# Performance work log

Hardware: AMD Instinct MI355X
Metric: run time of the kernel (lower is better)

## Reference

```python
import jax, jax.numpy as jnp
import numpy as np

B, CQ, CKV, E = 8, 256, 256, 256
H, W = 64, 64
HP, WP = 32, 32


def setup_inputs() -> dict:
    key = jax.random.key(0)
    ks = jax.random.split(key, 6)
    C = jax.random.normal(ks[0], (B, CQ, H, W), dtype=jnp.float32)
    P = jax.random.normal(ks[1], (B, CKV, HP, WP), dtype=jnp.float32)
    # 1x1 conv weights, kaiming-ish scale; stored as [out_ch, in_ch]
    theta_w = jax.random.normal(ks[2], (E, CQ), dtype=jnp.float32) * (1.0 / np.sqrt(CQ))
    phi_w = jax.random.normal(ks[3], (E, CKV), dtype=jnp.float32) * (1.0 / np.sqrt(CKV))
    g_w = jax.random.normal(ks[4], (E, CKV), dtype=jnp.float32) * (1.0 / np.sqrt(CKV))
    out_w = jax.random.normal(ks[5], (CQ, E), dtype=jnp.float32) * (1.0 / np.sqrt(E))
    return {"C": C, "P": P, "theta_w": theta_w, "phi_w": phi_w, "g_w": g_w, "out_w": out_w}


def reference(C, P, theta_w, phi_w, g_w, out_w):
    b, _, h, w = C.shape
    e = theta_w.shape[0]
    # 1x1 convs are channel GEMMs
    theta_C = jnp.einsum('bchw,ec->behw', C, theta_w).reshape(b, e, h * w)   # [B,E,Nq]
    phi_P = jnp.einsum('bchw,ec->behw', P, phi_w).reshape(b, e, -1)          # [B,E,Nkv]
    g_P = jnp.einsum('bchw,ec->behw', P, g_w).reshape(b, e, -1)              # [B,E,Nkv]
    attn = jnp.einsum('ben,bem->bnm', theta_C, phi_P) / (e ** 0.5)           # [B,Nq,Nkv]
    attn = jax.nn.softmax(attn, axis=-1)
    out = jnp.einsum('bem,bnm->ben', g_P, attn).reshape(b, e, h, w)          # [B,E,H,W]
    out = jnp.einsum('behw,ce->bchw', out, out_w)                            # [B,CQ,H,W]
    return jnp.concatenate([C, out], axis=1)
```

## Files before the change

kernel.cpp:

```cpp
#include <hip/hip_runtime.h>


typedef __attribute__((ext_vector_type(8))) short short8;
typedef __attribute__((ext_vector_type(16))) float f32x16;
typedef unsigned short ushort_t;

__device__ __forceinline__ unsigned short f2bf(float f) {
    unsigned int u = __float_as_uint(f);
    u += 0x7FFFu + ((u >> 16) & 1u);
    return (unsigned short)(u >> 16);
}
__device__ __forceinline__ unsigned int pack2bf(float a, float b) {
    return (unsigned int)f2bf(a) | ((unsigned int)f2bf(b) << 16);
}
__device__ __forceinline__ void gload16(const ushort_t* g, ushort_t* l) {
    __builtin_amdgcn_global_load_lds(
        (const __attribute__((address_space(1))) unsigned int*)g,
        (__attribute__((address_space(3))) unsigned int*)l, 16, 0, 0);
}
__device__ __forceinline__ f32x16 zero16() {
    f32x16 z;
#pragma unroll
    for (int i = 0; i < 16; ++i) z[i] = 0.f;
    return z;
}

__global__ __launch_bounds__(256) void prep_w(const float* __restrict__ thw,
                                              const float* __restrict__ phw,
                                              const float* __restrict__ ow,
                                              const float* __restrict__ gw,
                                              ushort_t* __restrict__ thc,
                                              ushort_t* __restrict__ phc,
                                              ushort_t* __restrict__ w2c) {
    int blk = blockIdx.x;
    int t = threadIdx.x;
    if (blk < 64) {
        int which = blk >> 5;
        int e0 = (blk & 31) * 8;
        const float* src = which ? phw : thw;
        ushort_t* dst = which ? phc : thc;
#pragma unroll
        for (int i = 0; i < 8; ++i) {
            int e = e0 + i, c = t;
            int idx = ((((e >> 5) * 16 + (c >> 4)) * 64 + ((c >> 3) & 1) * 32 + (e & 31)) << 3) + (c & 7);
            dst[idx] = f2bf(src[e * 256 + c]);
        }
    } else {
        int c0 = (blk - 64) * 8;
        float acc[8] = {};
        for (int e = 0; e < 256; ++e) {
            float g = gw[e * 256 + t];
#pragma unroll
            for (int i = 0; i < 8; ++i) acc[i] += ow[(c0 + i) * 256 + e] * g;
        }
#pragma unroll
        for (int i = 0; i < 8; ++i) {
            int c = c0 + i, k = t;
            int idx = ((((c >> 5) * 16 + (k >> 4)) * 64 + ((k >> 3) & 1) * 32 + (c & 31)) << 3) + (k & 7);
            w2c[idx] = f2bf(acc[i]);
        }
    }
}

__global__ __launch_bounds__(256, 4) void proj_all(const ushort_t* __restrict__ thc,
                                                   const ushort_t* __restrict__ phc,
                                                   const ushort_t* __restrict__ w2c,
                                                   const float* __restrict__ C,
                                                   const float* __restrict__ P,
                                                   ushort_t* __restrict__ thetaA,
                                                   ushort_t* __restrict__ phiA,
                                                   ushort_t* __restrict__ gVx) {
    __shared__ __align__(16) ushort_t Xc[16384];
    int blk = blockIdx.x;
    int tid = threadIdx.x, lane = tid & 63, wid = tid >> 6;
    int l31 = lane & 31, lh = lane >> 5;
    const int wq = wid & 1, we = wid >> 1;

    int role, b, nt, N;
    const ushort_t* Wc;
    const float* Xg;
    ushort_t* outp;
    float scale = 1.f;
    if (blk < 512) {
        role = 0; b = blk & 7; nt = blk >> 3;
        Wc = thc; Xg = C + (size_t)b * 1048576; outp = thetaA + (size_t)b * 1048576;
        N = 4096; scale = 1.4426950408889634f / 16.0f;
    } else if (blk < 640) {
        int r = blk - 512; role = 1; b = r & 7; nt = r >> 3;
        Wc = phc; Xg = P + (size_t)b * 262144; outp = phiA + (size_t)b * 262144;
        N = 1024;
    } else {
        int r = blk - 640; role = 2; b = r & 7; nt = r >> 3;
        Wc = w2c; Xg = P + (size_t)b * 262144; outp = gVx + (size_t)b * 262144;
        N = 1024;
    }

    {
        const float* Xb = Xg + nt * 64;
        const int q = lane;
        const int sq = q >> 5, sl = q & 31;
#pragma unroll
        for (int it = 0; it < 16; ++it) {
            int ch0 = wid * 4 + it * 16;
            float v0 = Xb[(size_t)(ch0 + 0) * N + q];
            float v1 = Xb[(size_t)(ch0 + 1) * N + q];
            float v2 = Xb[(size_t)(ch0 + 2) * N + q];
            float v3 = Xb[(size_t)(ch0 + 3) * N + q];
            uint2 w;
            w.x = pack2bf(v0, v1);
            w.y = pack2bf(v2, v3);
            int ks = ch0 >> 4;
            int slh = (ch0 >> 3) & 1;
            size_t a = ((size_t)(ks * 2 + sq) * 64 + slh * 32 + sl) * 8 + (ch0 & 7);
            *(uint2*)&Xc[a] = w;
        }
    }
    __syncthreads();

    const int n0 = nt * 64 + wq * 32;
    const int ncr = (n0 >> 5) * 16;

    f32x16 o[4];
#pragma unroll
    for (int f = 0; f < 4; ++f) o[f] = zero16();

#pragma unroll
    for (int ks = 0; ks < 16; ++ks) {
        short8 xf = *(const short8*)(Xc + ((size_t)(ks * 2 + wq) * 64 + lane) * 8);
#pragma unroll
        for (int f2 = 0; f2 < 4; ++f2) {
            int f = we * 4 + f2;
            short8 wf = *(const short8*)(Wc + ((size_t)(f * 16 + ks) * 64 + lane) * 8);
            o[f2] = __builtin_amdgcn_mfma_f32_32x32x16_bf16(wf, xf, o[f2], 0, 0, 0);
        }
    }

    if (role < 2) {
#pragma unroll
        for (int f2 = 0; f2 < 4; ++f2) {
            int f = we * 4 + f2;
#pragma unroll
            for (int rq = 0; rq < 4; ++rq) {
                uint2 st;
                st.x = pack2bf(o[f2][4 * rq + 0] * scale, o[f2][4 * rq + 1] * scale);
                st.y = pack2bf(o[f2][4 * rq + 2] * scale, o[f2][4 * rq + 3] * scale);
                size_t addr = ((size_t)(ncr + f * 2 + (rq >> 1)) * 64 + l31 + 32 * (rq & 1)) * 8 + 4 * lh;
                *(uint2*)(outp + addr) = st;
            }
        }
    } else {
        int kvq = (n0 >> 4) + (l31 >> 4);
        int lhw = 32 * ((l31 >> 3) & 1);
        int kl = l31 & 7;
#pragma unroll
        for (int f2 = 0; f2 < 4; ++f2) {
            int f = we * 4 + f2;
#pragma unroll
            for (int r2 = 0; r2 < 16; ++r2) {
                int crow = (r2 & 3) + 8 * (r2 >> 2) + 4 * lh;
                size_t addr = ((size_t)(f * 64 + kvq) * 64 + crow + lhw) * 8 + kl;
                outp[addr] = f2bf(o[f2][r2]);
            }
        }
    }
}

__global__ __launch_bounds__(512, 2) void attn14(const ushort_t* __restrict__ thetaA,
                                                 const ushort_t* __restrict__ phiA,
                                                 const ushort_t* __restrict__ gVx,
                                                 const float* __restrict__ Cf,
                                                 float* __restrict__ out) {
    const int b = blockIdx.x & 7, qt = blockIdx.x >> 3;
    const int tid = threadIdx.x, lane = tid & 63, wid = tid >> 6;
    const int l31 = lane & 31, lh = lane >> 5;
    const int qg = wid & 3, z = wid >> 2;

    __shared__ __align__(16) ushort_t smem[65536];
    __shared__ __align__(16) ushort_t Pl[2][8192];

    const ushort_t* thA = thetaA + (size_t)b * 1048576;
    const ushort_t* phA = phiA + (size_t)b * 262144;
    const ushort_t* gVb = gVx + (size_t)b * 262144;

    auto stageK = [&](int j) {
        if (wid < 4) {
            const ushort_t* src = phA + (size_t)j * 16384 + (size_t)wid * 4096 + lane * 8;
            ushort_t* dst = smem + (j & 1) * 16384 + wid * 4096;
#pragma unroll
            for (int i = 0; i < 8; ++i) gload16(src + i * 512, dst + i * 512);
        }
    };
    auto stageV = [&](int j) {
        if (wid >= 4) {
            int w = wid - 4;
#pragma unroll
            for (int q2 = 0; q2 < 2; ++q2) {
                int f = w * 2 + q2;
#pragma unroll
                for (int jj = 0; jj < 4; ++jj) {
                    const ushort_t* src = gVb + ((size_t)(f * 64 + j * 4 + jj) * 64 + lane) * 8;
                    ushort_t* dst = smem + 32768 + (j & 1) * 16384 + f * 2048 + jj * 512;
                    gload16(src, dst);
                }
            }
        }
    };

    stageK(0); stageV(0);

    short8 qf[16];
    {
        const int qcr = (qt * 4 + qg) * 16;
#pragma unroll
        for (int ks = 0; ks < 16; ++ks)
            qf[ks] = *(const short8*)(thA + ((size_t)(qcr + ks) * 64 + lane) * 8);
    }

    asm volatile("s_waitcnt vmcnt(0)" ::: "memory");
    __builtin_amdgcn_s_barrier();
    __builtin_amdgcn_sched_barrier(0);
    stageK(1);

    f32x16 s = zero16();
    {
        const ushort_t* Kb = smem + z * 8192;
#pragma unroll
        for (int ks = 0; ks < 16; ++ks) {
            short8 kf = *(const short8*)(Kb + (size_t)ks * 512 + lane * 8);
            s = __builtin_amdgcn_mfma_f32_32x32x16_bf16(kf, qf[ks], s, 0, 0, 0);
        }
    }

    f32x16 o[4];
#pragma unroll
    for (int f = 0; f < 4; ++f) o[f] = zero16();
    float rl = 0.f;

    const size_t cbase = (size_t)b * 1048576 + (size_t)qt * 128 + (size_t)l31 * 4;
    const size_t dofs = (size_t)b * 1048576;
    size_t cpo = 0;
    float4 cpv;

    for (int it = 0; it < 16; ++it) {
#pragma unroll
        for (int r = 0; r < 16; ++r) s[r] = __builtin_amdgcn_exp2f(s[r]);
        float t0 = (s[0] + s[1]) + (s[2] + s[3]);
        float t1 = (s[4] + s[5]) + (s[6] + s[7]);
        float t2 = (s[8] + s[9]) + (s[10] + s[11]);
        float t3 = (s[12] + s[13]) + (s[14] + s[15]);
        float ps = (t0 + t1) + (t2 + t3);
        ps += __shfl_xor(ps, 32);
        rl += ps;

        unsigned int a0 = pack2bf(s[0], s[1]),   b0 = pack2bf(s[4], s[5]);
        unsigned int a1 = pack2bf(s[2], s[3]),   b1 = pack2bf(s[6], s[7]);
        unsigned int a2 = pack2bf(s[8], s[9]),   b2 = pack2bf(s[12], s[13]);
        unsigned int a3 = pack2bf(s[10], s[11]), b3 = pack2bf(s[14], s[15]);
        asm volatile("v_permlane32_swap_b32 %0, %1" : "+v"(a0), "+v"(b0));
        asm volatile("v_permlane32_swap_b32 %0, %1" : "+v"(a1), "+v"(b1));
        asm volatile("v_permlane32_swap_b32 %0, %1" : "+v"(a2), "+v"(b2));
        asm volatile("v_permlane32_swap_b32 %0, %1" : "+v"(a3), "+v"(b3));
        union PW { unsigned int u[4]; short8 v; };
        PW pw0, pw1;
        pw0.u[0] = a0; pw0.u[1] = a1; pw0.u[2] = b0; pw0.u[3] = b1;
        pw1.u[0] = a2; pw1.u[1] = a3; pw1.u[2] = b2; pw1.u[3] = b3;
        ushort_t* Pw = &Pl[it & 1][0];
        *(short8*)(Pw + ((size_t)(qg * 4 + 2 * z + 0) * 64 + lane) * 8) = pw0.v;
        *(short8*)(Pw + ((size_t)(qg * 4 + 2 * z + 1) * 64 + lane) * 8) = pw1.v;

        if (it == 0) asm volatile("s_waitcnt vmcnt(0)" ::: "memory");
        else         asm volatile("s_waitcnt vmcnt(1)" ::: "memory");
        asm volatile("s_waitcnt lgkmcnt(0)" ::: "memory");
        __builtin_amdgcn_s_barrier();
        __builtin_amdgcn_sched_barrier(0);

        if (it > 0) *(float4*)(out + cpo + dofs) = cpv;
        if (it < 14) stageK(it + 2);
        if (it < 15) stageV(it + 1);
        __builtin_amdgcn_sched_barrier(0);
        cpo = cbase + (size_t)(it * 16 + 2 * wid + lh) * 4096;
        cpv = *(const float4*)(Cf + cpo);

        const ushort_t* Vb = smem + 32768 + (it & 1) * 16384 + z * 8192;
        const ushort_t* Kb = smem + ((it + 1) & 1) * 16384 + z * 8192;
        const ushort_t* Pr = &Pl[it & 1][0];
        __builtin_amdgcn_s_setprio(1);
        if (it < 15) {
            f32x16 sn = zero16();
#pragma unroll
            for (int j = 0; j < 4; ++j) {
                short8 pf = *(const short8*)(Pr + ((size_t)(qg * 4 + j) * 64 + lane) * 8);
#pragma unroll
                for (int fl = 0; fl < 4; ++fl) {
                    short8 vf = *(const short8*)(Vb + (size_t)fl * 2048 + j * 512 + lane * 8);
                    o[fl] = __builtin_amdgcn_mfma_f32_32x32x16_bf16(vf, pf, o[fl], 0, 0, 0);
                    int ks = j * 4 + fl;
                    short8 kf = *(const short8*)(Kb + (size_t)ks * 512 + lane * 8);
                    sn = __builtin_amdgcn_mfma_f32_32x32x16_bf16(kf, qf[ks], sn, 0, 0, 0);
                }
            }
            s = sn;
        } else {
#pragma unroll
            for (int j = 0; j < 4; ++j) {
                short8 pf = *(const short8*)(Pr + ((size_t)(qg * 4 + j) * 64 + lane) * 8);
#pragma unroll
                for (int fl = 0; fl < 4; ++fl) {
                    short8 vf = *(const short8*)(Vb + (size_t)fl * 2048 + j * 512 + lane * 8);
                    o[fl] = __builtin_amdgcn_mfma_f32_32x32x16_bf16(vf, pf, o[fl], 0, 0, 0);
                }
            }
        }
        __builtin_amdgcn_s_setprio(0);
        __builtin_amdgcn_sched_barrier(0);
    }

    *(float4*)(out + cpo + dofs) = cpv;

    __syncthreads();
    float* rlS = (float*)smem;
    if (lane < 32) rlS[(z * 4 + qg) * 32 + l31] = rl;
    __syncthreads();
    float inv = 1.f / (rlS[(0 * 4 + qg) * 32 + l31] + rlS[(1 * 4 + qg) * 32 + l31]);
    float* ob = out + (size_t)b * 2097152 + (size_t)256 * 4096 + qt * 128 + qg * 32 + l31;
#pragma unroll
    for (int fl = 0; fl < 4; ++fl) {
#pragma unroll
        for (int r = 0; r < 16; ++r) {
            int e = z * 128 + fl * 32 + (r & 3) + 8 * (r >> 2) + 4 * lh;
            ob[(size_t)e * 4096] = o[fl][r] * inv;
        }
    }
}


extern "C" void kernel_launch(void* const* d_in, const int* in_sizes, int n_in,
                              void* d_out, int out_size, void* d_ws, size_t ws_size,
                              hipStream_t stream) {
    const float* C       = (const float*)d_in[0];
    const float* P       = (const float*)d_in[1];
    const float* theta_w = (const float*)d_in[2];
    const float* phi_w   = (const float*)d_in[3];
    const float* g_w     = (const float*)d_in[4];
    const float* out_w   = (const float*)d_in[5];
    float* out = (float*)d_out;

    ushort_t* ws = (ushort_t*)d_ws;
    ushort_t* thetaA = ws;
    ushort_t* phiA   = ws + 8388608;
    ushort_t* gVx    = ws + 10485760;
    ushort_t* thWc   = ws + 12582912;
    ushort_t* phWc   = ws + 12648448;
    ushort_t* w2c    = ws + 12713984;

    prep_w<<<96, 256, 0, stream>>>(theta_w, phi_w, out_w, g_w, thWc, phWc, w2c);
    proj_all<<<768, 256, 0, stream>>>(thWc, phWc, w2c, C, P, thetaA, phiA, gVx);
    attn14<<<256, 512, 0, stream>>>(thetaA, phiA, gVx, C, out);
}
```

Before: 103.8 us.

## Warp-specialize attention kernel with dedicated producer waves for loads and C copy

Adds four producer waves to the attention block, raising it to 768 threads. These waves alone issue the K/V global-to-LDS staging and the copy of the C passthrough channels. The eight compute waves now only do softmax and MFMA work, and the aim is to take load-issue and copy instructions off their critical path. In exchange, launch_bounds drops the min-2-blocks hint, so register budget and occupancy may change. Producer waves also wait with vmcnt(2) at each barrier, which can add stalls if their loads lag.

```diff
diff --git a/kernel.cpp b/kernel.cpp
--- a/kernel.cpp
+++ b/kernel.cpp
@@ -165,15 +165,16 @@
     }
 }
 
-__global__ __launch_bounds__(512, 2) void attn14(const ushort_t* __restrict__ thetaA,
-                                                 const ushort_t* __restrict__ phiA,
-                                                 const ushort_t* __restrict__ gVx,
-                                                 const float* __restrict__ Cf,
-                                                 float* __restrict__ out) {
+__global__ __launch_bounds__(768) void attn15(const ushort_t* __restrict__ thetaA,
+                                              const ushort_t* __restrict__ phiA,
+                                              const ushort_t* __restrict__ gVx,
+                                              const float* __restrict__ Cf,
+                                              float* __restrict__ out) {
     const int b = blockIdx.x & 7, qt = blockIdx.x >> 3;
     const int tid = threadIdx.x, lane = tid & 63, wid = tid >> 6;
     const int l31 = lane & 31, lh = lane >> 5;
-    const int qg = wid & 3, z = wid >> 2;
+    const bool comp = wid < 8;
+    const int qg = wid & 3, z = (wid >> 2) & 1;
 
     __shared__ __align__(16) ushort_t smem[65536];
     __shared__ __align__(16) ushort_t Pl[2][8192];
@@ -183,24 +184,26 @@
     const ushort_t* gVb = gVx + (size_t)b * 262144;
 
     auto stageK = [&](int j) {
-        if (wid < 4) {
-            const ushort_t* src = phA + (size_t)j * 16384 + (size_t)wid * 4096 + lane * 8;
-            ushort_t* dst = smem + (j & 1) * 16384 + wid * 4096;
-#pragma unroll
-            for (int i = 0; i < 8; ++i) gload16(src + i * 512, dst + i * 512);
+        if (wid == 8 || wid == 9) {
+            int w = wid - 8;
+#pragma unroll
+            for (int i = 0; i < 16; ++i) {
+                int ch = w * 16 + i;
+                gload16(phA + (size_t)j * 16384 + (size_t)ch * 512 + lane * 8,
+                        smem + (j & 1) * 16384 + ch * 512);
+            }
         }
     };
     auto stageV = [&](int j) {
-        if (wid >= 4) {
-            int w = wid - 4;
-#pragma unroll
-            for (int q2 = 0; q2 < 2; ++q2) {
-                int f = w * 2 + q2;
+        if (wid == 10 || wid == 11) {
+            int w = wid - 10;
+#pragma unroll
+            for (int q2 = 0; q2 < 4; ++q2) {
+                int f = w * 4 + q2;
 #pragma unroll
                 for (int jj = 0; jj < 4; ++jj) {
-                    const ushort_t* src = gVb + ((size_t)(f * 64 + j * 4 + jj) * 64 + lane) * 8;
-                    ushort_t* dst = smem + 32768 + (j & 1) * 16384 + f * 2048 + jj * 512;
-                    gload16(src, dst);
+                    gload16(gVb + ((size_t)(f * 64 + j * 4 + jj) * 64 + lane) * 8,
+                            smem + 32768 + (j & 1) * 16384 + f * 2048 + jj * 512);
                 }
             }
         }
@@ -209,7 +212,7 @@
     stageK(0); stageV(0);
 
     short8 qf[16];
-    {
+    if (comp) {
         const int qcr = (qt * 4 + qg) * 16;
 #pragma unroll
         for (int ks = 0; ks < 16; ++ks)
@@ -222,7 +225,7 @@
     stageK(1);
 
     f32x16 s = zero16();
-    {
+    if (comp) {
         const ushort_t* Kb = smem + z * 8192;
 #pragma unroll
         for (int ks = 0; ks < 16; ++ks) {
@@ -236,99 +239,116 @@
     for (int f = 0; f < 4; ++f) o[f] = zero16();
     float rl = 0.f;
 
-    const size_t cbase = (size_t)b * 1048576 + (size_t)qt * 128 + (size_t)l31 * 4;
+    const size_t cbase = (size_t)b * 1048576 + (size_t)qt * 128;
     const size_t dofs = (size_t)b * 1048576;
-    size_t cpo = 0;
-    float4 cpv;
+    size_t cpo0 = 0, cpo1 = 0;
+    float4 cpv0, cpv1;
 
     for (int it = 0; it < 16; ++it) {
-#pragma unroll
-        for (int r = 0; r < 16; ++r) s[r] = __builtin_amdgcn_exp2f(s[r]);
-        float t0 = (s[0] + s[1]) + (s[2] + s[3]);
-        float t1 = (s[4] + s[5]) + (s[6] + s[7]);
-        float t2 = (s[8] + s[9]) + (s[10] + s[11]);
-        float t3 = (s[12] + s[13]) + (s[14] + s[15]);
-        float ps = (t0 + t1) + (t2 + t3);
-        ps += __shfl_xor(ps, 32);
-        rl += ps;
-
-        unsigned int a0 = pack2bf(s[0], s[1]),   b0 = pack2bf(s[4], s[5]);
-        unsigned int a1 = pack2bf(s[2], s[3]),   b1 = pack2bf(s[6], s[7]);
-        unsigned int a2 = pack2bf(s[8], s[9]),   b2 = pack2bf(s[12], s[13]);
-        unsigned int a3 = pack2bf(s[10], s[11]), b3 = pack2bf(s[14], s[15]);
-        asm volatile("v_permlane32_swap_b32 %0, %1" : "+v"(a0), "+v"(b0));
-        asm volatile("v_permlane32_swap_b32 %0, %1" : "+v"(a1), "+v"(b1));
-        asm volatile("v_permlane32_swap_b32 %0, %1" : "+v"(a2), "+v"(b2));
-        asm volatile("v_permlane32_swap_b32 %0, %1" : "+v"(a3), "+v"(b3));
-        union PW { unsigned int u[4]; short8 v; };
-        PW pw0, pw1;
-        pw0.u[0] = a0; pw0.u[1] = a1; pw0.u[2] = b0; pw0.u[3] = b1;
-        pw1.u[0] = a2; pw1.u[1] = a3; pw1.u[2] = b2; pw1.u[3] = b3;
-        ushort_t* Pw = &Pl[it & 1][0];
-        *(short8*)(Pw + ((size_t)(qg * 4 + 2 * z + 0) * 64 + lane) * 8) = pw0.v;
-        *(short8*)(Pw + ((size_t)(qg * 4 + 2 * z + 1) * 64 + lane) * 8) = pw1.v;
-
-        if (it == 0) asm volatile("s_waitcnt vmcnt(0)" ::: "memory");
-        else         asm volatile("s_waitcnt vmcnt(1)" ::: "memory");
-        asm volatile("s_waitcnt lgkmcnt(0)" ::: "memory");
+        if (comp) {
+#pragma unroll
+            for (int r = 0; r < 16; ++r) s[r] = __builtin_amdgcn_exp2f(s[r]);
+            float t0 = (s[0] + s[1]) + (s[2] + s[3]);
+            float t1 = (s[4] + s[5]) + (s[6] + s[7]);
+            float t2 = (s[8] + s[9]) + (s[10] + s[11]);
+            float t3 = (s[12] + s[13]) + (s[14] + s[15]);
+            float ps = (t0 + t1) + (t2 + t3);
+            ps += __shfl_xor(ps, 32);
+            rl += ps;
+
+            unsigned int a0 = pack2bf(s[0], s[1]),   b0 = pack2bf(s[4], s[5]);
+            unsigned int a1 = pack2bf(s[2], s[3]),   b1 = pack2bf(s[6], s[7]);
+            unsigned int a2 = pack2bf(s[8], s[9]),   b2 = pack2bf(s[12], s[13]);
+            unsigned int a3 = pack2bf(s[10], s[11]), b3 = pack2bf(s[14], s[15]);
+            asm volatile("v_permlane32_swap_b32 %0, %1" : "+v"(a0), "+v"(b0));
+            asm volatile("v_permlane32_swap_b32 %0, %1" : "+v"(a1), "+v"(b1));
+            asm volatile("v_permlane32_swap_b32 %0, %1" : "+v"(a2), "+v"(b2));
+            asm volatile("v_permlane32_swap_b32 %0, %1" : "+v"(a3), "+v"(b3));
+            union PW { unsigned int u[4]; short8 v; };
+            PW pw0, pw1;
+            pw0.u[0] = a0; pw0.u[1] = a1; pw0.u[2] = b0; pw0.u[3] = b1;
+            pw1.u[0] = a2; pw1.u[1] = a3; pw1.u[2] = b2; pw1.u[3] = b3;
+            ushort_t* Pw = &Pl[it & 1][0];
+            *(short8*)(Pw + ((size_t)(qg * 4 + 2 * z + 0) * 64 + lane) * 8) = pw0.v;
+            *(short8*)(Pw + ((size_t)(qg * 4 + 2 * z + 1) * 64 + lane) * 8) = pw1.v;
+            asm volatile("s_waitcnt lgkmcnt(0)" ::: "memory");
+        } else {
+            if (it == 0) asm volatile("s_waitcnt vmcnt(0)" ::: "memory");
+            else         asm volatile("s_waitcnt vmcnt(2)" ::: "memory");
+        }
         __builtin_amdgcn_s_barrier();
         __builtin_amdgcn_sched_barrier(0);
 
-        if (it > 0) *(float4*)(out + cpo + dofs) = cpv;
-        if (it < 14) stageK(it + 2);
-        if (it < 15) stageV(it + 1);
-        __builtin_amdgcn_sched_barrier(0);
-        cpo = cbase + (size_t)(it * 16 + 2 * wid + lh) * 4096;
-        cpv = *(const float4*)(Cf + cpo);
-
-        const ushort_t* Vb = smem + 32768 + (it & 1) * 16384 + z * 8192;
-        const ushort_t* Kb = smem + ((it + 1) & 1) * 16384 + z * 8192;
-        const ushort_t* Pr = &Pl[it & 1][0];
-        __builtin_amdgcn_s_setprio(1);
-        if (it < 15) {
-            f32x16 sn = zero16();
-#pragma unroll
-            for (int j = 0; j < 4; ++j) {
-                short8 pf = *(const short8*)(Pr + ((size_t)(qg * 4 + j) * 64 + lane) * 8);
-#pragma unroll
-                for (int fl = 0; fl < 4; ++fl) {
-                    short8 vf = *(const short8*)(Vb + (size_t)fl * 2048 + j * 512 + lane * 8);
-                    o[fl] = __builtin_amdgcn_mfma_f32_32x32x16_bf16(vf, pf, o[fl], 0, 0, 0);
-                    int ks = j * 4 + fl;
-                    short8 kf = *(const short8*)(Kb + (size_t)ks * 512 + lane * 8);
-                    sn = __builtin_amdgcn_mfma_f32_32x32x16_bf16(kf, qf[ks], sn, 0, 0, 0);
+        if (comp) {
+            const ushort_t* Vb = smem + 32768 + (it & 1) * 16384 + z * 8192;
+            const ushort_t* Kb = smem + ((it + 1) & 1) * 16384 + z * 8192;
+            const ushort_t* Pr = &Pl[it & 1][0];
+            __builtin_amdgcn_s_setprio(1);
+            if (it < 15) {
+                f32x16 sn = zero16();
+#pragma unroll
+                for (int j = 0; j < 4; ++j) {
+                    short8 pf = *(const short8*)(Pr + ((size_t)(qg * 4 + j) * 64 + lane) * 8);
+#pragma unroll
+                    for (int fl = 0; fl < 4; ++fl) {
+                        short8 vf = *(const short8*)(Vb + (size_t)fl * 2048 + j * 512 + lane * 8);
+                        o[fl] = __builtin_amdgcn_mfma_f32_32x32x16_bf16(vf, pf, o[fl], 0, 0, 0);
+                        int ks = j * 4 + fl;
+                        short8 kf = *(const short8*)(Kb + (size_t)ks * 512 + lane * 8);
+                        sn = __builtin_amdgcn_mfma_f32_32x32x16_bf16(kf, qf[ks], sn, 0, 0, 0);
+                    }
                 }
-            }
-            s = sn;
+                s = sn;
+            } else {
+#pragma unroll
+                for (int j = 0; j < 4; ++j) {
+                    short8 pf = *(const short8*)(Pr + ((size_t)(qg * 4 + j) * 64 + lane) * 8);
+#pragma unroll
+                    for (int fl = 0; fl < 4; ++fl) {
+                        short8 vf = *(const short8*)(Vb + (size_t)fl * 2048 + j * 512 + lane * 8);
+                        o[fl] = __builtin_amdgcn_mfma_f32_32x32x16_bf16(vf, pf, o[fl], 0, 0, 0);
+                    }
+                }
+            }
+            __builtin_amdgcn_s_setprio(0);
+            __builtin_amdgcn_sched_barrier(0);
         } else {
-#pragma unroll
-            for (int j = 0; j < 4; ++j) {
-                short8 pf = *(const short8*)(Pr + ((size_t)(qg * 4 + j) * 64 + lane) * 8);
-#pragma unroll
-                for (int fl = 0; fl < 4; ++fl) {
-                    short8 vf = *(const short8*)(Vb + (size_t)fl * 2048 + j * 512 + lane * 8);
-                    o[fl] = __builtin_amdgcn_mfma_f32_32x32x16_bf16(vf, pf, o[fl], 0, 0, 0);
-                }
-            }
-        }
-        __builtin_amdgcn_s_setprio(0);
-        __builtin_amdgcn_sched_barrier(0);
-    }
-
-    *(float4*)(out + cpo + dofs) = cpv;
+            if (it > 0) {
+                *(float4*)(out + cpo0 + dofs) = cpv0;
+                *(float4*)(out + cpo1 + dofs) = cpv1;
+            }
+            if (it < 14) stageK(it + 2);
+            if (it < 15) stageV(it + 1);
+            __builtin_amdgcn_sched_barrier(0);
+            int t2 = tid - 512;
+            int idx0 = it * 512 + t2;
+            int idx1 = idx0 + 256;
+            cpo0 = cbase + (size_t)(idx0 >> 5) * 4096 + (idx0 & 31) * 4;
+            cpo1 = cbase + (size_t)(idx1 >> 5) * 4096 + (idx1 & 31) * 4;
+            cpv0 = *(const float4*)(Cf + cpo0);
+            cpv1 = *(const float4*)(Cf + cpo1);
+        }
+    }
+
+    if (!comp) {
+        *(float4*)(out + cpo0 + dofs) = cpv0;
+        *(float4*)(out + cpo1 + dofs) = cpv1;
+    }
 
     __syncthreads();
     float* rlS = (float*)smem;
-    if (lane < 32) rlS[(z * 4 + qg) * 32 + l31] = rl;
+    if (comp && lane < 32) rlS[(z * 4 + qg) * 32 + l31] = rl;
     __syncthreads();
-    float inv = 1.f / (rlS[(0 * 4 + qg) * 32 + l31] + rlS[(1 * 4 + qg) * 32 + l31]);
-    float* ob = out + (size_t)b * 2097152 + (size_t)256 * 4096 + qt * 128 + qg * 32 + l31;
-#pragma unroll
-    for (int fl = 0; fl < 4; ++fl) {
-#pragma unroll
-        for (int r = 0; r < 16; ++r) {
-            int e = z * 128 + fl * 32 + (r & 3) + 8 * (r >> 2) + 4 * lh;
-            ob[(size_t)e * 4096] = o[fl][r] * inv;
+    if (comp) {
+        float inv = 1.f / (rlS[(0 * 4 + qg) * 32 + l31] + rlS[(1 * 4 + qg) * 32 + l31]);
+        float* ob = out + (size_t)b * 2097152 + (size_t)256 * 4096 + qt * 128 + qg * 32 + l31;
+#pragma unroll
+        for (int fl = 0; fl < 4; ++fl) {
+#pragma unroll
+            for (int r = 0; r < 16; ++r) {
+                int e = z * 128 + fl * 32 + (r & 3) + 8 * (r >> 2) + 4 * lh;
+                ob[(size_t)e * 4096] = o[fl][r] * inv;
+            }
         }
     }
 }
@@ -355,5 +375,5 @@
 
     prep_w<<<96, 256, 0, stream>>>(theta_w, phi_w, out_w, g_w, thWc, phWc, w2c);
     proj_all<<<768, 256, 0, stream>>>(thWc, phWc, w2c, C, P, thetaA, phiA, gVx);
-    attn14<<<256, 512, 0, stream>>>(thetaA, phiA, gVx, C, out);
-}
+    attn15<<<256, 768, 0, stream>>>(thetaA, phiA, gVx, C, out);
+}
```

After: 164.1 us. 58.1% more time.

## Move C passthrough copy into projection kernel and reuse own P fragments from registers

Applied to the files above, without the earlier changes.

The concatenated C half of the output is now written by the projection kernel, which already reads C to build theta, so the attention kernel no longer reloads and stores C inside its main loop. The attention loop also reorders its P·V k-chunks so each wave first uses the two P fragments it just computed in registers, and reads only the other wave's two fragments from LDS. The per-iteration memory wait is simplified to vmcnt(0). This removes a redundant global read of C and some LDS reads, but adds strided global stores to the projection kernel and changes the accumulation order.

```diff
diff --git a/kernel.cpp b/kernel.cpp
--- a/kernel.cpp
+++ b/kernel.cpp
@@ -69,7 +69,8 @@
                                                    const float* __restrict__ P,
                                                    ushort_t* __restrict__ thetaA,
                                                    ushort_t* __restrict__ phiA,
-                                                   ushort_t* __restrict__ gVx) {
+                                                   ushort_t* __restrict__ gVx,
+                                                   float* __restrict__ out) {
     __shared__ __align__(16) ushort_t Xc[16384];
     int blk = blockIdx.x;
     int tid = threadIdx.x, lane = tid & 63, wid = tid >> 6;
@@ -97,6 +98,7 @@
 
     {
         const float* Xb = Xg + nt * 64;
+        float* outC = (role == 0) ? out + (size_t)b * 2097152 + nt * 64 : nullptr;
         const int q = lane;
         const int sq = q >> 5, sl = q & 31;
 #pragma unroll
@@ -106,6 +108,12 @@
             float v1 = Xb[(size_t)(ch0 + 1) * N + q];
             float v2 = Xb[(size_t)(ch0 + 2) * N + q];
             float v3 = Xb[(size_t)(ch0 + 3) * N + q];
+            if (role == 0) {
+                outC[(size_t)(ch0 + 0) * 4096 + q] = v0;
+                outC[(size_t)(ch0 + 1) * 4096 + q] = v1;
+                outC[(size_t)(ch0 + 2) * 4096 + q] = v2;
+                outC[(size_t)(ch0 + 3) * 4096 + q] = v3;
+            }
             uint2 w;
             w.x = pack2bf(v0, v1);
             w.y = pack2bf(v2, v3);
@@ -165,10 +173,9 @@
     }
 }
 
-__global__ __launch_bounds__(512, 2) void attn14(const ushort_t* __restrict__ thetaA,
+__global__ __launch_bounds__(512, 2) void attn16(const ushort_t* __restrict__ thetaA,
                                                  const ushort_t* __restrict__ phiA,
                                                  const ushort_t* __restrict__ gVx,
-                                                 const float* __restrict__ Cf,
                                                  float* __restrict__ out) {
     const int b = blockIdx.x & 7, qt = blockIdx.x >> 3;
     const int tid = threadIdx.x, lane = tid & 63, wid = tid >> 6;
@@ -236,10 +243,7 @@
     for (int f = 0; f < 4; ++f) o[f] = zero16();
     float rl = 0.f;
 
-    const size_t cbase = (size_t)b * 1048576 + (size_t)qt * 128 + (size_t)l31 * 4;
-    const size_t dofs = (size_t)b * 1048576;
-    size_t cpo = 0;
-    float4 cpv;
+    union PW { unsigned int u[4]; short8 v; };
 
     for (int it = 0; it < 16; ++it) {
 #pragma unroll
@@ -260,7 +264,6 @@
         asm volatile("v_permlane32_swap_b32 %0, %1" : "+v"(a1), "+v"(b1));
         asm volatile("v_permlane32_swap_b32 %0, %1" : "+v"(a2), "+v"(b2));
         asm volatile("v_permlane32_swap_b32 %0, %1" : "+v"(a3), "+v"(b3));
-        union PW { unsigned int u[4]; short8 v; };
         PW pw0, pw1;
         pw0.u[0] = a0; pw0.u[1] = a1; pw0.u[2] = b0; pw0.u[3] = b1;
         pw1.u[0] = a2; pw1.u[1] = a3; pw1.u[2] = b2; pw1.u[3] = b3;
@@ -268,33 +271,34 @@
         *(short8*)(Pw + ((size_t)(qg * 4 + 2 * z + 0) * 64 + lane) * 8) = pw0.v;
         *(short8*)(Pw + ((size_t)(qg * 4 + 2 * z + 1) * 64 + lane) * 8) = pw1.v;
 
-        if (it == 0) asm volatile("s_waitcnt vmcnt(0)" ::: "memory");
-        else         asm volatile("s_waitcnt vmcnt(1)" ::: "memory");
+        asm volatile("s_waitcnt vmcnt(0)" ::: "memory");
         asm volatile("s_waitcnt lgkmcnt(0)" ::: "memory");
         __builtin_amdgcn_s_barrier();
         __builtin_amdgcn_sched_barrier(0);
 
-        if (it > 0) *(float4*)(out + cpo + dofs) = cpv;
         if (it < 14) stageK(it + 2);
         if (it < 15) stageV(it + 1);
-        __builtin_amdgcn_sched_barrier(0);
-        cpo = cbase + (size_t)(it * 16 + 2 * wid + lh) * 4096;
-        cpv = *(const float4*)(Cf + cpo);
 
         const ushort_t* Vb = smem + 32768 + (it & 1) * 16384 + z * 8192;
         const ushort_t* Kb = smem + ((it + 1) & 1) * 16384 + z * 8192;
         const ushort_t* Pr = &Pl[it & 1][0];
+        const int jo0 = 2 * z, jo1 = 2 * z + 1;
+        const int jf0 = 2 * (1 - z), jf1 = jf0 + 1;
         __builtin_amdgcn_s_setprio(1);
         if (it < 15) {
             f32x16 sn = zero16();
 #pragma unroll
-            for (int j = 0; j < 4; ++j) {
-                short8 pf = *(const short8*)(Pr + ((size_t)(qg * 4 + j) * 64 + lane) * 8);
+            for (int jj = 0; jj < 4; ++jj) {
+                int j = (jj == 0) ? jo0 : (jj == 1) ? jo1 : (jj == 2) ? jf0 : jf1;
+                short8 pf;
+                if (jj == 0)      pf = pw0.v;
+                else if (jj == 1) pf = pw1.v;
+                else              pf = *(const short8*)(Pr + ((size_t)(qg * 4 + j) * 64 + lane) * 8);
 #pragma unroll
                 for (int fl = 0; fl < 4; ++fl) {
                     short8 vf = *(const short8*)(Vb + (size_t)fl * 2048 + j * 512 + lane * 8);
                     o[fl] = __builtin_amdgcn_mfma_f32_32x32x16_bf16(vf, pf, o[fl], 0, 0, 0);
-                    int ks = j * 4 + fl;
+                    int ks = jj * 4 + fl;
                     short8 kf = *(const short8*)(Kb + (size_t)ks * 512 + lane * 8);
                     sn = __builtin_amdgcn_mfma_f32_32x32x16_bf16(kf, qf[ks], sn, 0, 0, 0);
                 }
@@ -302,8 +306,12 @@
             s = sn;
         } else {
 #pragma unroll
-            for (int j = 0; j < 4; ++j) {
-                short8 pf = *(const short8*)(Pr + ((size_t)(qg * 4 + j) * 64 + lane) * 8);
+            for (int jj = 0; jj < 4; ++jj) {
+                int j = (jj == 0) ? jo0 : (jj == 1) ? jo1 : (jj == 2) ? jf0 : jf1;
+                short8 pf;
+                if (jj == 0)      pf = pw0.v;
+                else if (jj == 1) pf = pw1.v;
+                else              pf = *(const short8*)(Pr + ((size_t)(qg * 4 + j) * 64 + lane) * 8);
 #pragma unroll
                 for (int fl = 0; fl < 4; ++fl) {
                     short8 vf = *(const short8*)(Vb + (size_t)fl * 2048 + j * 512 + lane * 8);
@@ -314,8 +322,6 @@
         __builtin_amdgcn_s_setprio(0);
         __builtin_amdgcn_sched_barrier(0);
     }
-
-    *(float4*)(out + cpo + dofs) = cpv;
 
     __syncthreads();
     float* rlS = (float*)smem;
@@ -354,6 +360,6 @@
     ushort_t* w2c    = ws + 12713984;
 
     prep_w<<<96, 256, 0, stream>>>(theta_w, phi_w, out_w, g_w, thWc, phWc, w2c);
-    proj_all<<<768, 256, 0, stream>>>(thWc, phWc, w2c, C, P, thetaA, phiA, gVx);
-    attn14<<<256, 512, 0, stream>>>(thetaA, phiA, gVx, C, out);
-}
+    proj_all<<<768, 256, 0, stream>>>(thWc, phWc, w2c, C, P, thetaA, phiA, gVx, out);
+    attn16<<<256, 512, 0, stream>>>(thetaA, phiA, gVx, out);
+}
```

New measurement: 105.1 us. No clear change (+1.3%).
